# Kernel optimization log

Hardware: AMD Instinct MI355X
Metric: run time of the kernel (lower is better)

Reference implementation:

```python
import jax, jax.numpy as jnp
import numpy as np

IN_DIM = 128
OUT_DIM = 128
D_MODEL = IN_DIM // 4        # mamba d_model = 32
D_STATE = 16
D_CONV = 4
EXPAND = 2
D_INNER = EXPAND * D_MODEL   # 64
DT_RANK = (D_MODEL + 15) // 16  # ceil(d_model/16) = 2
N_MIXERS = 3                 # shared + 2 experts (stacked on leading axis)
B, DD, HH, WW = 2, 16, 16, 16


def setup_inputs() -> dict:
    key = jax.random.key(0)
    ks = jax.random.split(key, 12)
    rn = lambda k, s, sc=0.05: jax.random.normal(k, s, dtype=jnp.float32) * sc
    M = N_MIXERS
    return {
        "x": jax.random.normal(ks[0], (B, IN_DIM, DD, HH, WW), dtype=jnp.float32),
        "dataset_id": jax.random.randint(ks[1], (B,), 0, 2),
        "ln_g": jnp.ones((M, IN_DIM), jnp.float32),
        "ln_b": jnp.zeros((M, IN_DIM), jnp.float32),
        "in_w": rn(ks[2], (M, 2 * D_INNER, D_MODEL)),
        "conv_w": rn(ks[3], (M, D_INNER, D_CONV), 0.2),
        "conv_b": rn(ks[4], (M, D_INNER), 0.1),
        "xp_w": rn(ks[5], (M, DT_RANK + 2 * D_STATE, D_INNER)),
        "dt_w": rn(ks[6], (M, D_INNER, DT_RANK), 0.2),
        "dt_b": rn(ks[7], (M, D_INNER), 0.1),
        "A_log": jnp.broadcast_to(jnp.log(jnp.arange(1, D_STATE + 1, dtype=jnp.float32)), (M, D_INNER, D_STATE)) + jnp.zeros((M, D_INNER, D_STATE), jnp.float32),
        "Dp": jnp.ones((M, D_INNER), jnp.float32),
        "out_w": rn(ks[8], (M, D_MODEL, D_INNER)),
        "proj_w": rn(ks[9], (M, OUT_DIM, IN_DIM)),
        "proj_b": jnp.zeros((M, OUT_DIM), jnp.float32),
        "skip": jnp.ones((M,), jnp.float32),
    }


def layernorm(x, g, b, eps=1e-5):
    mu = jnp.mean(x, -1, keepdims=True)
    var = jnp.mean((x - mu) ** 2, -1, keepdims=True)
    return (x - mu) * jax.lax.rsqrt(var + eps) * g + b


def mamba(xp, p):
    # Standard Mamba block: in_proj -> causal depthwise conv1d -> selective scan -> SiLU gate -> out_proj
    # xp: (B, L, d_model)
    Bb, L, _ = xp.shape
    xz = jnp.einsum('bld,ed->ble', xp, p["in_w"])            # (B,L,2*d_inner)
    xi, z = jnp.split(xz, 2, axis=-1)
    conv = jax.lax.conv_general_dilated(xi.transpose(0, 2, 1), p["conv_w"][:, None, :], (1,), [(D_CONV - 1, 0)], feature_group_count=D_INNER)
    xi = jax.nn.silu(conv + p["conv_b"][None, :, None]).transpose(0, 2, 1)  # (B,L,d_inner)
    dbc = jnp.einsum('bld,ed->ble', xi, p["xp_w"])
    dt_low = dbc[..., :DT_RANK]
    Bm = dbc[..., DT_RANK:DT_RANK + D_STATE]
    Cm = dbc[..., DT_RANK + D_STATE:]
    delta = jax.nn.softplus(jnp.einsum('blr,dr->bld', dt_low, p["dt_w"]) + p["dt_b"])  # (B,L,d_inner)
    A = -jnp.exp(p["A_log"])                                  # (d_inner, d_state)

    def step(h, inp):
        xt, dt, Bt, Ct = inp                                  # (B,di),(B,di),(B,ds),(B,ds)
        dA = jnp.exp(dt[..., None] * A)                       # (B,d_inner,d_state)
        h = dA * h + (dt * xt)[..., None] * Bt[:, None, :]
        return h, jnp.einsum('bds,bs->bd', h, Ct)

    h0 = jnp.zeros((Bb, D_INNER, D_STATE), xp.dtype)
    xs = (xi.transpose(1, 0, 2), delta.transpose(1, 0, 2), Bm.transpose(1, 0, 2), Cm.transpose(1, 0, 2))
    _, ys = jax.lax.scan(step, h0, xs)
    y = ys.transpose(1, 0, 2) + p["Dp"] * xi
    y = y * jax.nn.silu(z)
    return jnp.einsum('ble,de->bld', y, p["out_w"])


def mixer(x, p):
    # PetaloMixer pom_module='full': LN -> 4-way channel chunk -> shared Mamba + skip -> concat -> LN -> Linear
    Bb, C, Dd, Hh, Ww = x.shape
    L = Dd * Hh * Ww
    xf = x.reshape(Bb, C, L).transpose(0, 2, 1)               # (B,L,C)
    xn = layernorm(xf, p["ln_g"], p["ln_b"])
    parts = jnp.stack(jnp.split(xn, 4, axis=-1), 0)           # (4,B,L,d_model)
    outs = jax.vmap(lambda q: mamba(q, p))(parts) + p["skip"] * parts
    xm = jnp.concatenate([outs[i] for i in range(4)], -1)     # (B,L,C)
    xm = layernorm(xm, p["ln_g"], p["ln_b"])                  # same LayerNorm reused, as in torch code
    xpj = jnp.einsum('blc,oc->blo', xm, p["proj_w"]) + p["proj_b"]
    return xpj.transpose(0, 2, 1).reshape(Bb, OUT_DIM, Dd, Hh, Ww)


def _forward(x, dataset_id, params):
    shared = mixer(x, {k: v[0] for k, v in params.items()})
    # experts: compute both over full batch (vectorized), then per-sample select by dataset_id
    eouts = jax.vmap(lambda p: mixer(x, p))({k: v[1:] for k, v in params.items()})  # (2,B,out,D,H,W)
    ids = jnp.minimum(dataset_id, N_MIXERS - 2)               # clamp: min(m, n_experts-1)
    expert_out = eouts[ids, jnp.arange(x.shape[0])]
    return shared + expert_out                                # Dropout3d(p=0.2) is identity in eval mode


def reference(x, dataset_id, ln_g, ln_b, in_w, conv_w, conv_b, xp_w, dt_w, dt_b, A_log, Dp, out_w, proj_w, proj_b, skip):
    params = dict(ln_g=ln_g, ln_b=ln_b, in_w=in_w, conv_w=conv_w, conv_b=conv_b, xp_w=xp_w, dt_w=dt_w, dt_b=dt_b, A_log=A_log, Dp=Dp, out_w=out_w, proj_w=proj_w, proj_b=proj_b, skip=skip)
    return _forward(x, dataset_id, params)
```

## Files before the change

### kernel.cpp

```cpp
#include <hip/hip_runtime.h>
#include <math.h>

#define LSEQ 4096
#define CIN  128
#define DI   64
#define NS   16
#define NP   4
#define NJ   4
#define NSEQ 16
#define NC   128
#define LC   32
#define LOG2E 1.44269504f

__device__ __forceinline__ int mixer_of(const int* did, int j){
  if((j&1)==0) return 0;
  int d = did[j>>1];
  return 1 + (d < 1 ? d : 1);
}
__device__ __forceinline__ float silu_f(float x){ return x/(1.f+expf(-x)); }

__global__ __launch_bounds__(256) void k1_ln_inproj(
  const float* __restrict__ x, const int* __restrict__ did,
  const float* __restrict__ ln_g, const float* __restrict__ ln_b,
  const float* __restrict__ in_w,
  float* __restrict__ xnb, float* __restrict__ xzr, float* __restrict__ zb)
{
  const int j = blockIdx.y, b = j>>1, t = threadIdx.x;
  const int l0 = blockIdx.x*32;
  const int m = mixer_of(did, j);
  __shared__ float s_x[128][33];
  __shared__ float s_xn[32][132];
  __shared__ float s_mu[32], s_rs[32];

  for(int idx=t; idx<4096; idx+=256){
    int c = idx>>5, ll = idx&31;
    s_x[c][ll] = x[((size_t)b*CIN+c)*LSEQ + l0+ll];
  }
  float wreg[32];
  {
    const float4* wp = (const float4*)(in_w + (size_t)m*4096 + (size_t)(t&127)*32);
    #pragma unroll
    for(int i=0;i<8;i++){
      float4 v = wp[i];
      wreg[i*4+0]=v.x; wreg[i*4+1]=v.y; wreg[i*4+2]=v.z; wreg[i*4+3]=v.w;
    }
  }
  __syncthreads();

  {
    const int wv = t>>6, lane = t&63;
    const int g = lane&7, lw = lane>>3;
    const int ll = wv*8+lw;
    float sum=0.f;
    #pragma unroll
    for(int k=0;k<16;k++) sum += s_x[g*16+k][ll];
    sum += __shfl_xor(sum,1); sum += __shfl_xor(sum,2); sum += __shfl_xor(sum,4);
    float mu = sum*(1.f/128.f);
    float vs=0.f;
    #pragma unroll
    for(int k=0;k<16;k++){ float dv = s_x[g*16+k][ll]-mu; vs += dv*dv; }
    vs += __shfl_xor(vs,1); vs += __shfl_xor(vs,2); vs += __shfl_xor(vs,4);
    if(g==0){ s_mu[ll]=mu; s_rs[ll]=rsqrtf(vs*(1.f/128.f)+1e-5f); }
  }
  __syncthreads();

  for(int idx=t; idx<4096; idx+=256){
    int ll = idx>>7, c = idx&127;
    float xn = (s_x[c][ll]-s_mu[ll])*s_rs[ll]*ln_g[m*128+c] + ln_b[m*128+c];
    s_xn[ll][c] = xn;
    xnb[((size_t)j*LSEQ + l0+ll)*128 + c] = xn;
  }
  __syncthreads();

  const int e = t&127, hh = t>>7;
  for(int ll=hh*16; ll<hh*16+16; ++ll){
    #pragma unroll
    for(int q=0;q<4;q++){
      const float4* xr4 = (const float4*)(&s_xn[ll][q*32]);
      float acc=0.f;
      #pragma unroll
      for(int k4=0;k4<8;k4++){
        float4 xv = xr4[k4];
        acc += xv.x*wreg[k4*4+0] + xv.y*wreg[k4*4+1]
             + xv.z*wreg[k4*4+2] + xv.w*wreg[k4*4+3];
      }
      size_t base = ((size_t)(j*NP+q)*LSEQ + l0+ll)*64;
      if(e<64) xzr[base+e]=acc; else zb[base+e-64]=acc;
    }
  }
}

__global__ __launch_bounds__(256) void k2_conv_xproj_pe(
  const int* __restrict__ did,
  const float* __restrict__ conv_w, const float* __restrict__ conv_b,
  const float* __restrict__ xp_w, const float* __restrict__ dt_w, const float* __restrict__ dt_b,
  const float* __restrict__ A_log,
  const float* __restrict__ xzr, float* __restrict__ dxb,
  float* __restrict__ bmb, float* __restrict__ cmb,
  float* __restrict__ pb, float* __restrict__ eb)
{
  const int seq = blockIdx.y, j = seq>>2, t = threadIdx.x;
  const int chunk = blockIdx.x;
  const int l0 = chunk*32;
  const int m = mixer_of(did, j);
  const int d = t&63, r = t>>6;
  __shared__ float s_xi[32][64];
  __shared__ float s_dl[32][64];
  __shared__ float s_bS[32][16];
  __shared__ float s_dbc[32][2];
  __shared__ float s_cwT[4][64];
  __shared__ float s_cb[64], s_dtw[128], s_dtb[64];

  float lz[11];
  #pragma unroll
  for(int i=0;i<11;i++){
    int l = l0 + r*8 - 3 + i;
    lz[i] = (l>=0) ? xzr[((size_t)seq*LSEQ + l)*64 + d] : 0.f;
  }
  { int k=t>>6, dd=t&63; s_cwT[k][dd]=conv_w[m*256+dd*4+k]; }
  if(t<64){ s_cb[t]=conv_b[m*64+t]; s_dtb[t]=dt_b[m*64+t]; }
  if(t<128) s_dtw[t]=dt_w[m*128+t];
  __syncthreads();

  {
    float cw0=s_cwT[0][d], cw1=s_cwT[1][d], cw2=s_cwT[2][d], cw3=s_cwT[3][d], cb=s_cb[d];
    #pragma unroll
    for(int i=0;i<8;i++){
      float xc = cb + lz[i]*cw0 + lz[i+1]*cw1 + lz[i+2]*cw2 + lz[i+3]*cw3;
      s_xi[r*8+i][d] = silu_f(xc);
    }
  }

  float wreg[64];
  if(d<34){
    const float4* wp = (const float4*)(xp_w + (size_t)m*2176 + (size_t)d*64);
    #pragma unroll
    for(int k4=0;k4<16;k4++){
      float4 v = wp[k4];
      wreg[k4*4+0]=v.x; wreg[k4*4+1]=v.y; wreg[k4*4+2]=v.z; wreg[k4*4+3]=v.w;
    }
  }
  __syncthreads();

  if(d<34){
    #pragma unroll
    for(int ip=0; ip<4; ip++){
      int ll = r*8 + ip*2;
      const float4* xa=(const float4*)&s_xi[ll][0];
      const float4* xb=(const float4*)&s_xi[ll+1][0];
      float a0=0.f,a1=0.f,b0=0.f,b1=0.f;
      #pragma unroll
      for(int k=0;k<16;k+=2){
        float4 u=xa[k], u2=xa[k+1], v=xb[k], v2=xb[k+1];
        a0 += u.x *wreg[4*k+0]+u.y *wreg[4*k+1]+u.z *wreg[4*k+2]+u.w *wreg[4*k+3];
        a1 += u2.x*wreg[4*k+4]+u2.y*wreg[4*k+5]+u2.z*wreg[4*k+6]+u2.w*wreg[4*k+7];
        b0 += v.x *wreg[4*k+0]+v.y *wreg[4*k+1]+v.z *wreg[4*k+2]+v.w *wreg[4*k+3];
        b1 += v2.x*wreg[4*k+4]+v2.y*wreg[4*k+5]+v2.z*wreg[4*k+6]+v2.w*wreg[4*k+7];
      }
      float A=a0+a1, Bv=b0+b1;
      if(d<2){ s_dbc[ll][d]=A; s_dbc[ll+1][d]=Bv; }
      else if(d<18){
        s_bS[ll][d-2]=A; s_bS[ll+1][d-2]=Bv;
        bmb[((size_t)seq*LSEQ + l0+ll  )*16 + d-2]=A;
        bmb[((size_t)seq*LSEQ + l0+ll+1)*16 + d-2]=Bv;
      } else {
        cmb[((size_t)seq*LSEQ + l0+ll  )*16 + d-18]=A;
        cmb[((size_t)seq*LSEQ + l0+ll+1)*16 + d-18]=Bv;
      }
    }
  }
  __syncthreads();

  {
    float w0=s_dtw[d*2], w1=s_dtw[d*2+1], bb=s_dtb[d];
    #pragma unroll
    for(int i=0;i<8;i++){
      int ll=r*8+i;
      float dtv = s_dbc[ll][0]*w0 + s_dbc[ll][1]*w1 + bb;
      float dlv = dtv>20.f ? dtv : log1pf(expf(dtv));
      s_dl[ll][d]=dlv;
      float2 pk; pk.x=dlv; pk.y=s_xi[ll][d];
      *(float2*)(dxb + ((size_t)seq*LSEQ + l0+ll)*128 + d*2) = pk;
    }
  }
  __syncthreads();

  {
    const int sq = r;
    float as_q[4], as0;
    {
      const float* ap = A_log + (size_t)m*1024 + d*16;
      as0 = -expf(ap[0])*LOG2E;
      #pragma unroll
      for(int k=0;k<4;k++) as_q[k] = -expf(ap[sq*4+k])*LOG2E;
    }
    bool stl = true;
    #pragma unroll
    for(int k=0;k<4;k++){ float ex=(float)(sq*4+k+1)*as0; stl = stl && (fabsf(as_q[k]-ex) <= 1e-4f*fabsf(ex)); }
    const bool structured = (__ballot(stl) == ~0ull);

    float E[4] = {0.f,0.f,0.f,0.f};
    float Sdl = 0.f;

    #define PSTEP(i_, FAST_) { \
      float dl = s_dl[i_][d]; \
      float u  = dl * s_xi[i_][d]; \
      Sdl += dl; \
      const float4 bv = *(const float4*)(&s_bS[i_][sq*4]); \
      float bb[4]={bv.x,bv.y,bv.z,bv.w}; \
      float p[4]; \
      if(FAST_){ float q=exp2f(dl*as0); p[0]=exp2f(dl*as_q[0]); \
        p[1]=p[0]*q; p[2]=p[1]*q; p[3]=p[2]*q; \
      } else { _Pragma("unroll") for(int k=0;k<4;k++) p[k]=exp2f(dl*as_q[k]); } \
      _Pragma("unroll") for(int k=0;k<4;k++) E[k]=fmaf(p[k],E[k],u*bb[k]); }

    if(structured){
      #pragma unroll 4
      for(int i=0;i<LC;i++){ PSTEP(i,1) }
    } else {
      #pragma unroll 4
      for(int i=0;i<LC;i++){ PSTEP(i,0) }
    }
    #undef PSTEP

    size_t oo=(((size_t)seq*NC+chunk)*64+d)*16 + sq*4;
    *(float4*)(pb+oo) = make_float4(exp2f(Sdl*as_q[0]),exp2f(Sdl*as_q[1]),
                                    exp2f(Sdl*as_q[2]),exp2f(Sdl*as_q[3]));
    *(float4*)(eb+oo) = make_float4(E[0],E[1],E[2],E[3]);
  }
}

__global__ __launch_bounds__(256) void k3b_combine(
  float* p_hs, const float* __restrict__ eb)
{
  const int seq=blockIdx.y, q=blockIdx.x, t=threadIdx.x;
  const size_t elem = (size_t)q*256+t;
  #define OFF(c_) (((size_t)seq*NC+(c_))*1024 + elem)
  float pA[16],eA[16],pB[16],eB[16];
  #pragma unroll
  for(int k=0;k<16;k++){ pA[k]=p_hs[OFF(k)]; eA[k]=eb[OFF(k)]; }
  float h=0.f;
  for(int bt=0; bt<8; bt+=2){
    if(bt+1<8){
      #pragma unroll
      for(int k=0;k<16;k++){ pB[k]=p_hs[OFF((bt+1)*16+k)]; eB[k]=eb[OFF((bt+1)*16+k)]; }
    }
    #pragma unroll
    for(int k=0;k<16;k++){ p_hs[OFF(bt*16+k)]=h; h=fmaf(pA[k],h,eA[k]); }
    if(bt+2<8){
      #pragma unroll
      for(int k=0;k<16;k++){ pA[k]=p_hs[OFF((bt+2)*16+k)]; eA[k]=eb[OFF((bt+2)*16+k)]; }
    }
    #pragma unroll
    for(int k=0;k<16;k++){ p_hs[OFF((bt+1)*16+k)]=h; h=fmaf(pB[k],h,eB[k]); }
  }
  #undef OFF
}

__global__ __launch_bounds__(256) void k3c4_scan_outproj(
  const int* __restrict__ did, const float* __restrict__ A_log, const float* __restrict__ Dp,
  const float* __restrict__ dxb,
  const float* __restrict__ bmb, const float* __restrict__ cmb,
  const float* __restrict__ zb, const float* __restrict__ hsb,
  const float* __restrict__ out_w, const float* __restrict__ skipv,
  const float* __restrict__ xnb, float* __restrict__ xmb)
{
  const int seq=blockIdx.y, j=seq>>2, p=seq&3, t=threadIdx.x;
  const int wave=t>>6, d=t&63;
  const int cl=wave>>1, sh=wave&1, sh8=sh*8;
  const int chunk=blockIdx.x*2+cl;
  const int l0=blockIdx.x*2*LC;
  const int m=mixer_of(did,j);
  __shared__ float s_b[2*LC*NS];
  __shared__ float s_c[2*LC*NS];
  __shared__ float s_y0[64*64];
  __shared__ float s_y1[64*64];
  {
    const float4* bsrc=(const float4*)(bmb + ((size_t)seq*LSEQ + l0)*NS);
    const float4* csrc=(const float4*)(cmb + ((size_t)seq*LSEQ + l0)*NS);
    ((float4*)s_b)[t]=bsrc[t];
    ((float4*)s_c)[t]=csrc[t];
  }
  float as_h[8], as0;
  {
    const float* ap = A_log + (size_t)m*1024 + d*16;
    as0 = -expf(ap[0])*LOG2E;
    #pragma unroll
    for(int k=0;k<8;k++) as_h[k] = -expf(ap[sh8+k])*LOG2E;
  }
  bool stl = true;
  #pragma unroll
  for(int k=0;k<8;k++){ float ex=(float)(sh8+k+1)*as0; stl = stl && (fabsf(as_h[k]-ex) <= 1e-4f*fabsf(ex)); }
  const bool structured = (__ballot(stl) == ~0ull);

  const float dpv2 = (sh==0) ? Dp[m*64+d] : 0.f;
  float h[8];
  {
    const float4* hp=(const float4*)(hsb + (((size_t)seq*NC+chunk)*64+d)*16 + sh8);
    float4 v0=hp[0], v1=hp[1];
    h[0]=v0.x; h[1]=v0.y; h[2]=v0.z; h[3]=v0.w;
    h[4]=v1.x; h[5]=v1.y; h[6]=v1.z; h[7]=v1.w;
  }
  const float2* dxp=(const float2*)(dxb + ((size_t)seq*LSEQ + (size_t)chunk*LC)*128);
  float* s_yw = sh ? s_y1 : s_y0;
  __syncthreads();

  #define CSTEP(i_, dx_, FAST_) { \
    float dl=dx_.x, xv=dx_.y; float u=dl*xv; \
    const float4* bq=(const float4*)(s_b + cl*(LC*NS) + (i_)*NS + sh8); \
    const float4* cq=(const float4*)(s_c + cl*(LC*NS) + (i_)*NS + sh8); \
    float4 b0=bq[0],b1=bq[1],c0=cq[0],c1=cq[1]; \
    float bb[8]={b0.x,b0.y,b0.z,b0.w, b1.x,b1.y,b1.z,b1.w}; \
    float cc[8]={c0.x,c0.y,c0.z,c0.w, c1.x,c1.y,c1.z,c1.w}; \
    float pz[8]; \
    if(FAST_){ float q=exp2f(dl*as0); pz[0]=exp2f(dl*as_h[0]); \
      _Pragma("unroll") for(int k=1;k<8;k++) pz[k]=pz[k-1]*q; \
    } else { _Pragma("unroll") for(int k=0;k<8;k++) pz[k]=exp2f(dl*as_h[k]); } \
    float ya=0.f, yb2=0.f; \
    _Pragma("unroll") for(int k=0;k<8;k++){ \
      h[k]=fmaf(pz[k],h[k],u*bb[k]); \
      float hv=h[k]*cc[k]; \
      if(k&1) yb2+=hv; else ya+=hv; } \
    float y=ya+yb2; y=fmaf(dpv2,xv,y); \
    s_yw[(cl*LC+(i_))*64 + d]=y; }

  #define CLOOP(FAST_) { \
    float2 dxw[4]; \
    _Pragma("unroll") for(int k=0;k<4;k++) dxw[k]=dxp[k*64+d]; \
    for(int ii=0;ii<LC;ii+=4){ \
      float2 c0w=dxw[0],c1w=dxw[1],c2w=dxw[2],c3w=dxw[3]; \
      if(ii+4<LC){ _Pragma("unroll") for(int k=0;k<4;k++) dxw[k]=dxp[(ii+4+k)*64+d]; } \
      CSTEP(ii+0,c0w,FAST_); CSTEP(ii+1,c1w,FAST_); CSTEP(ii+2,c2w,FAST_); CSTEP(ii+3,c3w,FAST_); } }

  if(structured){ CLOOP(1) } else { CLOOP(0) }
  #undef CLOOP
  #undef CSTEP

  __syncthreads();
  {
    const float* zp = zb + ((size_t)seq*LSEQ + l0)*64;
    #pragma unroll
    for(int it=0; it<16; ++it){
      int idx = t + it*256;
      float ysum = s_y0[idx] + s_y1[idx];
      s_y0[idx] = ysum * silu_f(zp[idx]);
    }
  }
  const int o=t&31, grp=t>>5;
  float wreg[64];
  {
    const float4* wp=(const float4*)(out_w + (size_t)m*2048 + (size_t)o*64);
    #pragma unroll
    for(int k4=0;k4<16;k4++){
      float4 v=wp[k4];
      wreg[k4*4+0]=v.x; wreg[k4*4+1]=v.y; wreg[k4*4+2]=v.z; wreg[k4*4+3]=v.w;
    }
  }
  const float sk=skipv[m];
  __syncthreads();
  for(int ll=grp; ll<64; ll+=8){
    const float4* ya=(const float4*)&s_y0[ll*64];
    float a0=0.f,a1=0.f;
    #pragma unroll
    for(int k=0;k<16;k+=2){
      float4 u=ya[k], u2=ya[k+1];
      a0 += u.x *wreg[4*k+0]+u.y *wreg[4*k+1]+u.z *wreg[4*k+2]+u.w *wreg[4*k+3];
      a1 += u2.x*wreg[4*k+4]+u2.y*wreg[4*k+5]+u2.z*wreg[4*k+6]+u2.w*wreg[4*k+7];
    }
    size_t xidx=((size_t)j*LSEQ + l0+ll)*128 + p*32 + o;
    xmb[xidx]=(a0+a1) + sk*xnb[xidx];
  }
}

__global__ __launch_bounds__(256) void k5_ln2_proj(
  const int* __restrict__ did, const float* __restrict__ ln_g, const float* __restrict__ ln_b,
  const float* __restrict__ proj_w, const float* __restrict__ proj_b,
  const float* __restrict__ xmb, float* __restrict__ out)
{
  const int b=blockIdx.y, l0=blockIdx.x*16, t=threadIdx.x;
  const int eh = t>>7, local = t&127;
  const int j = 2*b+eh;
  const int m = mixer_of(did, j);
  __shared__ float s_xn[2][16][132];
  __shared__ float s_comb[16][132];
  __shared__ float s_murs[2][16][2];

  for(int idx=local; idx<2048; idx+=128){
    int ll=idx>>7, c=idx&127;
    s_xn[eh][ll][c] = xmb[((size_t)j*LSEQ + l0+ll)*128 + c];
  }
  __syncthreads();
  {
    const int lane = t&63;
    const int g = lane&7, lw = lane>>3;
    const int ll = ((t>>6)&1)*8 + lw;
    float sum=0.f;
    #pragma unroll
    for(int k=0;k<16;k++) sum += s_xn[eh][ll][g*16+k];
    sum += __shfl_xor(sum,1); sum += __shfl_xor(sum,2); sum += __shfl_xor(sum,4);
    float mu = sum*(1.f/128.f);
    float vs=0.f;
    #pragma unroll
    for(int k=0;k<16;k++){ float dv=s_xn[eh][ll][g*16+k]-mu; vs+=dv*dv; }
    vs += __shfl_xor(vs,1); vs += __shfl_xor(vs,2); vs += __shfl_xor(vs,4);
    if(g==0){ s_murs[eh][ll][0]=mu; s_murs[eh][ll][1]=rsqrtf(vs*(1.f/128.f)+1e-5f); }
  }
  __syncthreads();
  for(int idx=local; idx<2048; idx+=128){
    int ll=idx>>7, c=idx&127;
    float xn=(s_xn[eh][ll][c]-s_murs[eh][ll][0])*s_murs[eh][ll][1]*ln_g[m*128+c]+ln_b[m*128+c];
    s_xn[eh][ll][c]=xn;
  }
  __syncthreads();
  float acc[16];
  #pragma unroll
  for(int ll=0;ll<16;ll++) acc[ll]=0.f;
  {
    const float4* pw4 = (const float4*)(proj_w + (size_t)m*16384 + (size_t)local*128);
    #pragma unroll 4
    for(int c4=0;c4<32;c4++){
      float4 w = pw4[c4];
      int c = c4*4;
      #pragma unroll
      for(int ll=0;ll<16;ll++){
        acc[ll] += w.x*s_xn[eh][ll][c] + w.y*s_xn[eh][ll][c+1]
                 + w.z*s_xn[eh][ll][c+2] + w.w*s_xn[eh][ll][c+3];
      }
    }
  }
  float pb_v = proj_b[m*128+local];
  if(eh==0){
    #pragma unroll
    for(int ll=0;ll<16;ll++) s_comb[ll][local]=acc[ll]+pb_v;
  }
  __syncthreads();
  if(eh==1){
    #pragma unroll
    for(int ll=0;ll<16;ll++) s_comb[ll][local]+=acc[ll]+pb_v;
  }
  __syncthreads();
  for(int idx=t; idx<2048; idx+=256){
    int o=idx>>4, ll=idx&15;
    out[((size_t)b*128+o)*LSEQ + l0+ll] = s_comb[ll][o];
  }
}

extern "C" void kernel_launch(void* const* d_in, const int* in_sizes, int n_in,
                              void* d_out, int out_size, void* d_ws, size_t ws_size,
                              hipStream_t stream) {
  const float* x      = (const float*)d_in[0];
  const int*   did    = (const int*)d_in[1];
  const float* ln_g   = (const float*)d_in[2];
  const float* ln_b   = (const float*)d_in[3];
  const float* in_w   = (const float*)d_in[4];
  const float* conv_w = (const float*)d_in[5];
  const float* conv_b = (const float*)d_in[6];
  const float* xp_w   = (const float*)d_in[7];
  const float* dt_w   = (const float*)d_in[8];
  const float* dt_b   = (const float*)d_in[9];
  const float* A_log  = (const float*)d_in[10];
  const float* Dp     = (const float*)d_in[11];
  const float* out_w  = (const float*)d_in[12];
  const float* proj_w = (const float*)d_in[13];
  const float* proj_b = (const float*)d_in[14];
  const float* skipv  = (const float*)d_in[15];
  float* out = (float*)d_out;
  float* ws  = (float*)d_ws;

  float* xnb = ws;
  float* xzr = xnb + (size_t)NJ*LSEQ*128;
  float* zb  = xzr + (size_t)NSEQ*LSEQ*64;
  float* dxb = zb  + (size_t)NSEQ*LSEQ*64;
  float* bmb = dxb + (size_t)NSEQ*LSEQ*128;
  float* cmb = bmb + (size_t)NSEQ*LSEQ*16;
  float* xmb = cmb + (size_t)NSEQ*LSEQ*16;
  float* pb  = xmb + (size_t)NJ*LSEQ*128;
  float* eb  = pb  + (size_t)NSEQ*NC*1024;
  float* hsb = pb;

  hipLaunchKernelGGL(k1_ln_inproj, dim3(LSEQ/32,NJ), dim3(256), 0, stream,
                     x,did,ln_g,ln_b,in_w,xnb,xzr,zb);
  hipLaunchKernelGGL(k2_conv_xproj_pe, dim3(NC,NSEQ), dim3(256), 0, stream,
                     did,conv_w,conv_b,xp_w,dt_w,dt_b,A_log,xzr,dxb,bmb,cmb,pb,eb);
  hipLaunchKernelGGL(k3b_combine, dim3(4,NSEQ), dim3(256), 0, stream, pb,eb);
  hipLaunchKernelGGL(k3c4_scan_outproj, dim3(NC/2,NSEQ), dim3(256), 0, stream,
                     did,A_log,Dp,dxb,bmb,cmb,zb,hsb,out_w,skipv,xnb,xmb);
  hipLaunchKernelGGL(k5_ln2_proj, dim3(LSEQ/16,2), dim3(256), 0, stream,
                     did,ln_g,ln_b,proj_w,proj_b,xmb,out);
}
```

Before: 132.2 us.

## Split dt projection via wave shuffles and quarter state in chunked scan

In the conv/x-proj kernel, the two dt-rank outputs are now computed with wave-wide shuffle reductions right after the conv. This removes one barrier and lets all 256 threads compute the 32 B/C projections, where only 34 of every 64 lanes did work before. The precomputed dl*x product is kept in shared memory so the local scan step reads one float2. The scan/out-proj kernel now gives each block one chunk, with four waves each holding a quarter of the state. This doubles the grid and halves per-thread state registers, but the y reduction now sums four partial buffers in shared memory.

```diff
diff --git a/kernel.cpp b/kernel.cpp
--- a/kernel.cpp
+++ b/kernel.cpp
@@ -104,12 +104,13 @@
   const int l0 = chunk*32;
   const int m = mixer_of(did, j);
   const int d = t&63, r = t>>6;
-  __shared__ float s_xi[32][64];
-  __shared__ float s_dl[32][64];
-  __shared__ float s_bS[32][16];
-  __shared__ float s_dbc[32][2];
-  __shared__ float s_cwT[4][64];
-  __shared__ float s_cb[64], s_dtw[128], s_dtb[64];
+  __shared__ float  s_xi[32][64];
+  __shared__ float2 s_dx[32][64];
+  __shared__ float  s_bS[32][16];
+  __shared__ float  s_dbc[32][2];
+  __shared__ float  s_cwT[4][64];
+  __shared__ float  s_xpw01[2][64];
+  __shared__ float  s_cb[64], s_dtw[128], s_dtb[64];
 
   float lz[11];
   #pragma unroll
@@ -119,21 +120,11 @@
   }
   { int k=t>>6, dd=t&63; s_cwT[k][dd]=conv_w[m*256+dd*4+k]; }
   if(t<64){ s_cb[t]=conv_b[m*64+t]; s_dtb[t]=dt_b[m*64+t]; }
-  if(t<128) s_dtw[t]=dt_w[m*128+t];
-  __syncthreads();
-
-  {
-    float cw0=s_cwT[0][d], cw1=s_cwT[1][d], cw2=s_cwT[2][d], cw3=s_cwT[3][d], cb=s_cb[d];
-    #pragma unroll
-    for(int i=0;i<8;i++){
-      float xc = cb + lz[i]*cw0 + lz[i+1]*cw1 + lz[i+2]*cw2 + lz[i+3]*cw3;
-      s_xi[r*8+i][d] = silu_f(xc);
-    }
-  }
-
+  if(t<128){ s_dtw[t]=dt_w[m*128+t]; s_xpw01[t>>6][t&63]=xp_w[m*2176 + t]; }
+  const int o2 = t&31, rg = t>>5;
   float wreg[64];
-  if(d<34){
-    const float4* wp = (const float4*)(xp_w + (size_t)m*2176 + (size_t)d*64);
+  {
+    const float4* wp = (const float4*)(xp_w + (size_t)m*2176 + (size_t)(2+o2)*64);
     #pragma unroll
     for(int k4=0;k4<16;k4++){
       float4 v = wp[k4];
@@ -142,10 +133,55 @@
   }
   __syncthreads();
 
-  if(d<34){
-    #pragma unroll
-    for(int ip=0; ip<4; ip++){
-      int ll = r*8 + ip*2;
+  float xir[8];
+  {
+    float cw0=s_cwT[0][d], cw1=s_cwT[1][d], cw2=s_cwT[2][d], cw3=s_cwT[3][d], cb=s_cb[d];
+    #pragma unroll
+    for(int i=0;i<8;i++){
+      float xc = cb + lz[i]*cw0 + lz[i+1]*cw1 + lz[i+2]*cw2 + lz[i+3]*cw3;
+      xir[i] = silu_f(xc);
+      s_xi[r*8+i][d] = xir[i];
+    }
+  }
+
+  {
+    float pr[8];
+    #pragma unroll
+    for(int i=0;i<8;i++){
+      float p0 = xir[i]*s_xpw01[0][d];
+      float p1 = xir[i]*s_xpw01[1][d];
+      float q0 = p0 + __shfl_xor(p0,1);
+      float q1 = p1 + __shfl_xor(p1,1);
+      pr[i] = (d&1) ? q1 : q0;
+    }
+    #pragma unroll
+    for(int off=2; off<64; off<<=1){
+      #pragma unroll
+      for(int i=0;i<8;i++) pr[i] += __shfl_xor(pr[i], off);
+    }
+    if(d<2){
+      #pragma unroll
+      for(int i=0;i<8;i++) s_dbc[r*8+i][d] = pr[i];
+    }
+  }
+  __syncthreads();
+
+  {
+    float w0=s_dtw[d*2], w1=s_dtw[d*2+1], bb=s_dtb[d];
+    #pragma unroll
+    for(int i=0;i<8;i++){
+      int ll=r*8+i;
+      float dtv = s_dbc[ll][0]*w0 + s_dbc[ll][1]*w1 + bb;
+      float dlv = dtv>20.f ? dtv : log1pf(expf(dtv));
+      s_dx[ll][d] = make_float2(dlv, dlv*xir[i]);
+      *(float2*)(dxb + ((size_t)seq*LSEQ + l0+ll)*128 + d*2) = make_float2(dlv, xir[i]);
+    }
+  }
+
+  {
+    #pragma unroll
+    for(int ip=0; ip<2; ip++){
+      int ll = rg*4 + ip*2;
       const float4* xa=(const float4*)&s_xi[ll][0];
       const float4* xb=(const float4*)&s_xi[ll+1][0];
       float a0=0.f,a1=0.f,b0=0.f,b1=0.f;
@@ -158,29 +194,14 @@
         b1 += v2.x*wreg[4*k+4]+v2.y*wreg[4*k+5]+v2.z*wreg[4*k+6]+v2.w*wreg[4*k+7];
       }
       float A=a0+a1, Bv=b0+b1;
-      if(d<2){ s_dbc[ll][d]=A; s_dbc[ll+1][d]=Bv; }
-      else if(d<18){
-        s_bS[ll][d-2]=A; s_bS[ll+1][d-2]=Bv;
-        bmb[((size_t)seq*LSEQ + l0+ll  )*16 + d-2]=A;
-        bmb[((size_t)seq*LSEQ + l0+ll+1)*16 + d-2]=Bv;
+      if(o2<16){
+        s_bS[ll][o2]=A; s_bS[ll+1][o2]=Bv;
+        bmb[((size_t)seq*LSEQ + l0+ll  )*16 + o2]=A;
+        bmb[((size_t)seq*LSEQ + l0+ll+1)*16 + o2]=Bv;
       } else {
-        cmb[((size_t)seq*LSEQ + l0+ll  )*16 + d-18]=A;
-        cmb[((size_t)seq*LSEQ + l0+ll+1)*16 + d-18]=Bv;
+        cmb[((size_t)seq*LSEQ + l0+ll  )*16 + o2-16]=A;
+        cmb[((size_t)seq*LSEQ + l0+ll+1)*16 + o2-16]=Bv;
       }
-    }
-  }
-  __syncthreads();
-
-  {
-    float w0=s_dtw[d*2], w1=s_dtw[d*2+1], bb=s_dtb[d];
-    #pragma unroll
-    for(int i=0;i<8;i++){
-      int ll=r*8+i;
-      float dtv = s_dbc[ll][0]*w0 + s_dbc[ll][1]*w1 + bb;
-      float dlv = dtv>20.f ? dtv : log1pf(expf(dtv));
-      s_dl[ll][d]=dlv;
-      float2 pk; pk.x=dlv; pk.y=s_xi[ll][d];
-      *(float2*)(dxb + ((size_t)seq*LSEQ + l0+ll)*128 + d*2) = pk;
     }
   }
   __syncthreads();
@@ -203,16 +224,16 @@
     float Sdl = 0.f;
 
     #define PSTEP(i_, FAST_) { \
-      float dl = s_dl[i_][d]; \
-      float u  = dl * s_xi[i_][d]; \
+      float2 du = s_dx[i_][d]; \
+      float dl = du.x, u = du.y; \
       Sdl += dl; \
       const float4 bv = *(const float4*)(&s_bS[i_][sq*4]); \
-      float bb[4]={bv.x,bv.y,bv.z,bv.w}; \
-      float p[4]; \
-      if(FAST_){ float q=exp2f(dl*as0); p[0]=exp2f(dl*as_q[0]); \
-        p[1]=p[0]*q; p[2]=p[1]*q; p[3]=p[2]*q; \
-      } else { _Pragma("unroll") for(int k=0;k<4;k++) p[k]=exp2f(dl*as_q[k]); } \
-      _Pragma("unroll") for(int k=0;k<4;k++) E[k]=fmaf(p[k],E[k],u*bb[k]); }
+      float p_[4]; \
+      if(FAST_){ float q=exp2f(dl*as0); p_[0]=exp2f(dl*as_q[0]); \
+        p_[1]=p_[0]*q; p_[2]=p_[1]*q; p_[3]=p_[2]*q; \
+      } else { _Pragma("unroll") for(int k=0;k<4;k++) p_[k]=exp2f(dl*as_q[k]); } \
+      E[0]=fmaf(p_[0],E[0],u*bv.x); E[1]=fmaf(p_[1],E[1],u*bv.y); \
+      E[2]=fmaf(p_[2],E[2],u*bv.z); E[3]=fmaf(p_[3],E[3],u*bv.w); }
 
     if(structured){
       #pragma unroll 4
@@ -266,63 +287,56 @@
   const float* __restrict__ xnb, float* __restrict__ xmb)
 {
   const int seq=blockIdx.y, j=seq>>2, p=seq&3, t=threadIdx.x;
-  const int wave=t>>6, d=t&63;
-  const int cl=wave>>1, sh=wave&1, sh8=sh*8;
-  const int chunk=blockIdx.x*2+cl;
-  const int l0=blockIdx.x*2*LC;
+  const int sq=t>>6, d=t&63;
+  const int chunk=blockIdx.x;
+  const int l0=chunk*LC;
   const int m=mixer_of(did,j);
-  __shared__ float s_b[2*LC*NS];
-  __shared__ float s_c[2*LC*NS];
-  __shared__ float s_y0[64*64];
-  __shared__ float s_y1[64*64];
+  __shared__ float s_b[LC*NS];
+  __shared__ float s_c[LC*NS];
+  __shared__ float s_y[4][LC*64];
   {
     const float4* bsrc=(const float4*)(bmb + ((size_t)seq*LSEQ + l0)*NS);
     const float4* csrc=(const float4*)(cmb + ((size_t)seq*LSEQ + l0)*NS);
-    ((float4*)s_b)[t]=bsrc[t];
-    ((float4*)s_c)[t]=csrc[t];
-  }
-  float as_h[8], as0;
+    if(t<128) ((float4*)s_b)[t]=bsrc[t];
+    else      ((float4*)s_c)[t-128]=csrc[t-128];
+  }
+  float as_q[4], as0;
   {
     const float* ap = A_log + (size_t)m*1024 + d*16;
     as0 = -expf(ap[0])*LOG2E;
     #pragma unroll
-    for(int k=0;k<8;k++) as_h[k] = -expf(ap[sh8+k])*LOG2E;
+    for(int k=0;k<4;k++) as_q[k] = -expf(ap[sq*4+k])*LOG2E;
   }
   bool stl = true;
   #pragma unroll
-  for(int k=0;k<8;k++){ float ex=(float)(sh8+k+1)*as0; stl = stl && (fabsf(as_h[k]-ex) <= 1e-4f*fabsf(ex)); }
+  for(int k=0;k<4;k++){ float ex=(float)(sq*4+k+1)*as0; stl = stl && (fabsf(as_q[k]-ex) <= 1e-4f*fabsf(ex)); }
   const bool structured = (__ballot(stl) == ~0ull);
 
-  const float dpv2 = (sh==0) ? Dp[m*64+d] : 0.f;
-  float h[8];
-  {
-    const float4* hp=(const float4*)(hsb + (((size_t)seq*NC+chunk)*64+d)*16 + sh8);
-    float4 v0=hp[0], v1=hp[1];
+  const float dpv = (sq==0) ? Dp[m*64+d] : 0.f;
+  float h[4];
+  {
+    const float4 v0 = *(const float4*)(hsb + (((size_t)seq*NC+chunk)*64+d)*16 + sq*4);
     h[0]=v0.x; h[1]=v0.y; h[2]=v0.z; h[3]=v0.w;
-    h[4]=v1.x; h[5]=v1.y; h[6]=v1.z; h[7]=v1.w;
-  }
-  const float2* dxp=(const float2*)(dxb + ((size_t)seq*LSEQ + (size_t)chunk*LC)*128);
-  float* s_yw = sh ? s_y1 : s_y0;
+  }
+  const float2* dxp=(const float2*)(dxb + ((size_t)seq*LSEQ + l0)*128);
+  float* s_yw = &s_y[sq][0];
   __syncthreads();
 
   #define CSTEP(i_, dx_, FAST_) { \
     float dl=dx_.x, xv=dx_.y; float u=dl*xv; \
-    const float4* bq=(const float4*)(s_b + cl*(LC*NS) + (i_)*NS + sh8); \
-    const float4* cq=(const float4*)(s_c + cl*(LC*NS) + (i_)*NS + sh8); \
-    float4 b0=bq[0],b1=bq[1],c0=cq[0],c1=cq[1]; \
-    float bb[8]={b0.x,b0.y,b0.z,b0.w, b1.x,b1.y,b1.z,b1.w}; \
-    float cc[8]={c0.x,c0.y,c0.z,c0.w, c1.x,c1.y,c1.z,c1.w}; \
-    float pz[8]; \
-    if(FAST_){ float q=exp2f(dl*as0); pz[0]=exp2f(dl*as_h[0]); \
-      _Pragma("unroll") for(int k=1;k<8;k++) pz[k]=pz[k-1]*q; \
-    } else { _Pragma("unroll") for(int k=0;k<8;k++) pz[k]=exp2f(dl*as_h[k]); } \
-    float ya=0.f, yb2=0.f; \
-    _Pragma("unroll") for(int k=0;k<8;k++){ \
-      h[k]=fmaf(pz[k],h[k],u*bb[k]); \
-      float hv=h[k]*cc[k]; \
-      if(k&1) yb2+=hv; else ya+=hv; } \
-    float y=ya+yb2; y=fmaf(dpv2,xv,y); \
-    s_yw[(cl*LC+(i_))*64 + d]=y; }
+    const float4 bv = *(const float4*)(s_b + (i_)*NS + sq*4); \
+    const float4 cv = *(const float4*)(s_c + (i_)*NS + sq*4); \
+    float pz[4]; \
+    if(FAST_){ float q=exp2f(dl*as0); pz[0]=exp2f(dl*as_q[0]); \
+      pz[1]=pz[0]*q; pz[2]=pz[1]*q; pz[3]=pz[2]*q; \
+    } else { _Pragma("unroll") for(int k=0;k<4;k++) pz[k]=exp2f(dl*as_q[k]); } \
+    h[0]=fmaf(pz[0],h[0],u*bv.x); h[1]=fmaf(pz[1],h[1],u*bv.y); \
+    h[2]=fmaf(pz[2],h[2],u*bv.z); h[3]=fmaf(pz[3],h[3],u*bv.w); \
+    float ya = h[0]*cv.x + h[2]*cv.z; \
+    float yb2 = h[1]*cv.y + h[3]*cv.w; \
+    float y = ya + yb2; \
+    y = fmaf(dpv, xv, y); \
+    s_yw[(i_)*64 + d] = y; }
 
   #define CLOOP(FAST_) { \
     float2 dxw[4]; \
@@ -340,10 +354,10 @@
   {
     const float* zp = zb + ((size_t)seq*LSEQ + l0)*64;
     #pragma unroll
-    for(int it=0; it<16; ++it){
+    for(int it=0; it<8; ++it){
       int idx = t + it*256;
-      float ysum = s_y0[idx] + s_y1[idx];
-      s_y0[idx] = ysum * silu_f(zp[idx]);
+      float ysum = s_y[0][idx] + s_y[1][idx] + s_y[2][idx] + s_y[3][idx];
+      s_y[0][idx] = ysum * silu_f(zp[idx]);
     }
   }
   const int o=t&31, grp=t>>5;
@@ -358,8 +372,8 @@
   }
   const float sk=skipv[m];
   __syncthreads();
-  for(int ll=grp; ll<64; ll+=8){
-    const float4* ya=(const float4*)&s_y0[ll*64];
+  for(int ll=grp; ll<LC; ll+=8){
+    const float4* ya=(const float4*)&s_y[0][ll*64];
     float a0=0.f,a1=0.f;
     #pragma unroll
     for(int k=0;k<16;k+=2){
@@ -483,7 +497,7 @@
   hipLaunchKernelGGL(k2_conv_xproj_pe, dim3(NC,NSEQ), dim3(256), 0, stream,
                      did,conv_w,conv_b,xp_w,dt_w,dt_b,A_log,xzr,dxb,bmb,cmb,pb,eb);
   hipLaunchKernelGGL(k3b_combine, dim3(4,NSEQ), dim3(256), 0, stream, pb,eb);
-  hipLaunchKernelGGL(k3c4_scan_outproj, dim3(NC/2,NSEQ), dim3(256), 0, stream,
+  hipLaunchKernelGGL(k3c4_scan_outproj, dim3(NC,NSEQ), dim3(256), 0, stream,
                      did,A_log,Dp,dxb,bmb,cmb,zb,hsb,out_w,skipv,xnb,xmb);
   hipLaunchKernelGGL(k5_ln2_proj, dim3(LSEQ/16,2), dim3(256), 0, stream,
                      did,ln_g,ln_b,proj_w,proj_b,xmb,out);
```

New measurement: 140.6 us. +6.3%, slower.

## Compute dt projection via wavefront shuffle reduction and use hardware exp2/rcp/log intrinsics

Applied to the files above, without the earlier changes.

Restructures the conv/x-projection kernel. The two dt_low rows of the x projection are now computed with a per-wave shuffle reduction straight from the conv outputs held in registers, so softplus and the dx store can run before the B/C projection. The B/C projection is remapped onto all 256 threads (32 outputs by 8 row groups) instead of leaving threads with d>=34 idle, and one barrier is removed. expf, exp2f, log1pf and division are replaced by raw AMD hardware exp2/log/rcp intrinsics in silu, softplus and the scan steps, which trades some accuracy and denormal handling for fewer instructions.

```diff
diff --git a/kernel.cpp b/kernel.cpp
--- a/kernel.cpp
+++ b/kernel.cpp
@@ -11,13 +11,20 @@
 #define NC   128
 #define LC   32
 #define LOG2E 1.44269504f
+#define LN2   0.6931471806f
 
 __device__ __forceinline__ int mixer_of(const int* did, int j){
   if((j&1)==0) return 0;
   int d = did[j>>1];
   return 1 + (d < 1 ? d : 1);
 }
-__device__ __forceinline__ float silu_f(float x){ return x/(1.f+expf(-x)); }
+__device__ __forceinline__ float fexp2(float x){ return __builtin_amdgcn_exp2f(x); }
+__device__ __forceinline__ float silu_f(float x){
+  return x*__builtin_amdgcn_rcpf(1.f + fexp2(-x*LOG2E));
+}
+__device__ __forceinline__ float softplus_f(float x){
+  return x>20.f ? x : LN2*__builtin_amdgcn_logf(1.f + fexp2(x*LOG2E));
+}
 
 __global__ __launch_bounds__(256) void k1_ln_inproj(
   const float* __restrict__ x, const int* __restrict__ did,
@@ -104,12 +111,13 @@
   const int l0 = chunk*32;
   const int m = mixer_of(did, j);
   const int d = t&63, r = t>>6;
-  __shared__ float s_xi[32][64];
-  __shared__ float s_dl[32][64];
-  __shared__ float s_bS[32][16];
-  __shared__ float s_dbc[32][2];
-  __shared__ float s_cwT[4][64];
-  __shared__ float s_cb[64], s_dtw[128], s_dtb[64];
+  __shared__ float  s_xi[32][64];
+  __shared__ float  s_dl[32][64];
+  __shared__ float  s_bS[32][16];
+  __shared__ float  s_dbc[32][2];
+  __shared__ float  s_cwT[4][64];
+  __shared__ float  s_xpw01[2][64];
+  __shared__ float  s_cb[64], s_dtw[128], s_dtb[64];
 
   float lz[11];
   #pragma unroll
@@ -119,21 +127,11 @@
   }
   { int k=t>>6, dd=t&63; s_cwT[k][dd]=conv_w[m*256+dd*4+k]; }
   if(t<64){ s_cb[t]=conv_b[m*64+t]; s_dtb[t]=dt_b[m*64+t]; }
-  if(t<128) s_dtw[t]=dt_w[m*128+t];
-  __syncthreads();
-
-  {
-    float cw0=s_cwT[0][d], cw1=s_cwT[1][d], cw2=s_cwT[2][d], cw3=s_cwT[3][d], cb=s_cb[d];
-    #pragma unroll
-    for(int i=0;i<8;i++){
-      float xc = cb + lz[i]*cw0 + lz[i+1]*cw1 + lz[i+2]*cw2 + lz[i+3]*cw3;
-      s_xi[r*8+i][d] = silu_f(xc);
-    }
-  }
-
+  if(t<128){ s_dtw[t]=dt_w[m*128+t]; s_xpw01[t>>6][t&63]=xp_w[m*2176 + t]; }
+  const int o2 = t&31, rg = t>>5;
   float wreg[64];
-  if(d<34){
-    const float4* wp = (const float4*)(xp_w + (size_t)m*2176 + (size_t)d*64);
+  {
+    const float4* wp = (const float4*)(xp_w + (size_t)m*2176 + (size_t)(2+o2)*64);
     #pragma unroll
     for(int k4=0;k4<16;k4++){
       float4 v = wp[k4];
@@ -142,10 +140,55 @@
   }
   __syncthreads();
 
-  if(d<34){
-    #pragma unroll
-    for(int ip=0; ip<4; ip++){
-      int ll = r*8 + ip*2;
+  float xir[8];
+  {
+    float cw0=s_cwT[0][d], cw1=s_cwT[1][d], cw2=s_cwT[2][d], cw3=s_cwT[3][d], cb=s_cb[d];
+    #pragma unroll
+    for(int i=0;i<8;i++){
+      float xc = cb + lz[i]*cw0 + lz[i+1]*cw1 + lz[i+2]*cw2 + lz[i+3]*cw3;
+      xir[i] = silu_f(xc);
+      s_xi[r*8+i][d] = xir[i];
+    }
+  }
+
+  {
+    float pr[8];
+    #pragma unroll
+    for(int i=0;i<8;i++){
+      float p0 = xir[i]*s_xpw01[0][d];
+      float p1 = xir[i]*s_xpw01[1][d];
+      float q0 = p0 + __shfl_xor(p0,1);
+      float q1 = p1 + __shfl_xor(p1,1);
+      pr[i] = (d&1) ? q1 : q0;
+    }
+    #pragma unroll
+    for(int off=2; off<64; off<<=1){
+      #pragma unroll
+      for(int i=0;i<8;i++) pr[i] += __shfl_xor(pr[i], off);
+    }
+    if(d<2){
+      #pragma unroll
+      for(int i=0;i<8;i++) s_dbc[r*8+i][d] = pr[i];
+    }
+  }
+  __syncthreads();
+
+  {
+    float w0=s_dtw[d*2], w1=s_dtw[d*2+1], bb=s_dtb[d];
+    #pragma unroll
+    for(int i=0;i<8;i++){
+      int ll=r*8+i;
+      float dtv = s_dbc[ll][0]*w0 + s_dbc[ll][1]*w1 + bb;
+      float dlv = softplus_f(dtv);
+      s_dl[ll][d] = dlv;
+      *(float2*)(dxb + ((size_t)seq*LSEQ + l0+ll)*128 + d*2) = make_float2(dlv, xir[i]);
+    }
+  }
+
+  {
+    #pragma unroll
+    for(int ip=0; ip<2; ip++){
+      int ll = rg*4 + ip*2;
       const float4* xa=(const float4*)&s_xi[ll][0];
       const float4* xb=(const float4*)&s_xi[ll+1][0];
       float a0=0.f,a1=0.f,b0=0.f,b1=0.f;
@@ -158,29 +201,14 @@
         b1 += v2.x*wreg[4*k+4]+v2.y*wreg[4*k+5]+v2.z*wreg[4*k+6]+v2.w*wreg[4*k+7];
       }
       float A=a0+a1, Bv=b0+b1;
-      if(d<2){ s_dbc[ll][d]=A; s_dbc[ll+1][d]=Bv; }
-      else if(d<18){
-        s_bS[ll][d-2]=A; s_bS[ll+1][d-2]=Bv;
-        bmb[((size_t)seq*LSEQ + l0+ll  )*16 + d-2]=A;
-        bmb[((size_t)seq*LSEQ + l0+ll+1)*16 + d-2]=Bv;
+      if(o2<16){
+        s_bS[ll][o2]=A; s_bS[ll+1][o2]=Bv;
+        bmb[((size_t)seq*LSEQ + l0+ll  )*16 + o2]=A;
+        bmb[((size_t)seq*LSEQ + l0+ll+1)*16 + o2]=Bv;
       } else {
-        cmb[((size_t)seq*LSEQ + l0+ll  )*16 + d-18]=A;
-        cmb[((size_t)seq*LSEQ + l0+ll+1)*16 + d-18]=Bv;
+        cmb[((size_t)seq*LSEQ + l0+ll  )*16 + o2-16]=A;
+        cmb[((size_t)seq*LSEQ + l0+ll+1)*16 + o2-16]=Bv;
       }
-    }
-  }
-  __syncthreads();
-
-  {
-    float w0=s_dtw[d*2], w1=s_dtw[d*2+1], bb=s_dtb[d];
-    #pragma unroll
-    for(int i=0;i<8;i++){
-      int ll=r*8+i;
-      float dtv = s_dbc[ll][0]*w0 + s_dbc[ll][1]*w1 + bb;
-      float dlv = dtv>20.f ? dtv : log1pf(expf(dtv));
-      s_dl[ll][d]=dlv;
-      float2 pk; pk.x=dlv; pk.y=s_xi[ll][d];
-      *(float2*)(dxb + ((size_t)seq*LSEQ + l0+ll)*128 + d*2) = pk;
     }
   }
   __syncthreads();
@@ -207,12 +235,12 @@
       float u  = dl * s_xi[i_][d]; \
       Sdl += dl; \
       const float4 bv = *(const float4*)(&s_bS[i_][sq*4]); \
-      float bb[4]={bv.x,bv.y,bv.z,bv.w}; \
-      float p[4]; \
-      if(FAST_){ float q=exp2f(dl*as0); p[0]=exp2f(dl*as_q[0]); \
-        p[1]=p[0]*q; p[2]=p[1]*q; p[3]=p[2]*q; \
-      } else { _Pragma("unroll") for(int k=0;k<4;k++) p[k]=exp2f(dl*as_q[k]); } \
-      _Pragma("unroll") for(int k=0;k<4;k++) E[k]=fmaf(p[k],E[k],u*bb[k]); }
+      float p_[4]; \
+      if(FAST_){ float q=fexp2(dl*as0); p_[0]=fexp2(dl*as_q[0]); \
+        p_[1]=p_[0]*q; p_[2]=p_[1]*q; p_[3]=p_[2]*q; \
+      } else { _Pragma("unroll") for(int k=0;k<4;k++) p_[k]=fexp2(dl*as_q[k]); } \
+      E[0]=fmaf(p_[0],E[0],u*bv.x); E[1]=fmaf(p_[1],E[1],u*bv.y); \
+      E[2]=fmaf(p_[2],E[2],u*bv.z); E[3]=fmaf(p_[3],E[3],u*bv.w); }
 
     if(structured){
       #pragma unroll 4
@@ -224,8 +252,8 @@
     #undef PSTEP
 
     size_t oo=(((size_t)seq*NC+chunk)*64+d)*16 + sq*4;
-    *(float4*)(pb+oo) = make_float4(exp2f(Sdl*as_q[0]),exp2f(Sdl*as_q[1]),
-                                    exp2f(Sdl*as_q[2]),exp2f(Sdl*as_q[3]));
+    *(float4*)(pb+oo) = make_float4(fexp2(Sdl*as_q[0]),fexp2(Sdl*as_q[1]),
+                                    fexp2(Sdl*as_q[2]),fexp2(Sdl*as_q[3]));
     *(float4*)(eb+oo) = make_float4(E[0],E[1],E[2],E[3]);
   }
 }
@@ -313,9 +341,9 @@
     float bb[8]={b0.x,b0.y,b0.z,b0.w, b1.x,b1.y,b1.z,b1.w}; \
     float cc[8]={c0.x,c0.y,c0.z,c0.w, c1.x,c1.y,c1.z,c1.w}; \
     float pz[8]; \
-    if(FAST_){ float q=exp2f(dl*as0); pz[0]=exp2f(dl*as_h[0]); \
+    if(FAST_){ float q=fexp2(dl*as0); pz[0]=fexp2(dl*as_h[0]); \
       _Pragma("unroll") for(int k=1;k<8;k++) pz[k]=pz[k-1]*q; \
-    } else { _Pragma("unroll") for(int k=0;k<8;k++) pz[k]=exp2f(dl*as_h[k]); } \
+    } else { _Pragma("unroll") for(int k=0;k<8;k++) pz[k]=fexp2(dl*as_h[k]); } \
     float ya=0.f, yb2=0.f; \
     _Pragma("unroll") for(int k=0;k<8;k++){ \
       h[k]=fmaf(pz[k],h[k],u*bb[k]); \
```

Result: faster. 120.4 us (-9.0%).
